# Kernel optimization log

Hardware: AMD Instinct MI355X
Metric: run time of the kernel (lower is better)

The kernel has to match this reference:

```python
import jax, jax.numpy as jnp
import numpy as np
import math

B, S, D, P = 128, 512, 1024, 32
TEMP, BETA = 0.1, 0.4

def _lin_init(k, din, dout):
    k1, k2 = jax.random.split(k)
    s = 1.0 / math.sqrt(din)
    W = jax.random.uniform(k1, (din, dout), minval=-s, maxval=s, dtype=jnp.float32)
    b = jax.random.uniform(k2, (dout,), minval=-s, maxval=s, dtype=jnp.float32)
    return W, b

def setup_inputs():
    key = jax.random.key(0)
    ks = jax.random.split(key, 20)
    inp = {
        'x_head': jax.random.normal(ks[0], (B, D), dtype=jnp.float32),
        'x_rel': jax.random.normal(ks[1], (B, S, D), dtype=jnp.float32),
        'x_tail': jax.random.normal(ks[2], (B, S, D), dtype=jnp.float32),
        'x_mask': (jax.random.uniform(ks[3], (B, S)) < 0.9).astype(jnp.float32),
        'x_img': jax.random.normal(ks[4], (B, D), dtype=jnp.float32),
    }
    names = [('wf1', 2 * D, D), ('wf2', D, D), ('wk', D, D), ('wv', D, D),
             ('wp', D, D), ('wiq', D, D), ('whq', D, D), ('wlt', D, D),
             ('wli', D, D), ('wltr', D, D), ('wgt', D, D), ('wgi', D, D)]
    for i, (nm, din, dout) in enumerate(names):
        W, b = _lin_init(ks[5 + i], din, dout)
        inp[nm] = W
        inp['b' + nm[1:]] = b
    return inp

def reference(x_head, x_rel, x_tail, x_mask, x_img,
              wf1, bf1, wf2, bf2, wk, bk, wv, bv, wp, bp,
              wiq, biq, whq, bhq, wlt, blt, wli, bli,
              wltr, bltr, wgt, bgt, wgi, bgi):
    # reltail feature combine: MLP(cat[tail, rel]) residual onto tail (eval: no dropout)
    feat = jnp.concatenate([x_tail, x_rel], axis=-1)            # [B,S,2D]
    h = jax.nn.leaky_relu(feat @ wf1 + bf1, negative_slope=0.01)
    x_reltail = x_tail + (h @ wf2 + bf2)                        # [B,S,D]
    keys = x_reltail @ wk + bk                                  # [B,S,D]
    values = x_reltail @ wv + bv                                # [B,S,D]
    iq = x_img @ wiq + biq                                      # [B,D]
    hq = x_head @ whq + bhq                                     # [B,D]
    inv_sqrt_d = 1.0 / math.sqrt(D)
    s1 = jnp.einsum('bd,bsd->bs', iq, keys) * inv_sqrt_d        # [B,S]
    s2 = jnp.einsum('bd,bsd->bs', hq, keys) * inv_sqrt_d
    neg_inf = jnp.finfo(s1.dtype).min
    valid = x_mask > 0.01
    s1 = jnp.where(valid, s1, neg_inf)
    s2 = jnp.where(valid, s2, neg_inf)
    scores = (s1 * BETA + s2 * (1.0 - BETA)) / TEMP
    attn = jax.nn.softmax(scores, axis=-1)                      # [B,S]
    # top-p sparsify: keep only the P largest weights (no renormalization)
    _, top_idx = jax.lax.top_k(attn, P)                         # [B,P]
    top_mask = jnp.zeros_like(attn).at[jnp.arange(B)[:, None], top_idx].set(1.0)
    attn = attn * top_mask
    ctx = jnp.einsum('bs,bsd->bd', attn, values)                # [B,D]
    x_triple = ctx @ wp + bp
    # gated projection combine
    text_out = x_head @ wlt + blt
    img_out = x_img @ wli + bli
    triple_out = x_triple @ wltr + bltr
    text_gate = jax.nn.sigmoid(x_head @ wgt + bgt)
    img_gate = jax.nn.sigmoid(x_img @ wgi + bgi)
    return triple_out + text_out * text_gate + img_out * img_gate
```

## Files before the change

### kernel.cpp

```cpp
#include <hip/hip_runtime.h>
#include <math.h>


typedef short bf16x8 __attribute__((ext_vector_type(8)));
typedef float f32x4 __attribute__((ext_vector_type(4)));

typedef const __attribute__((address_space(1))) void* gp_t;
typedef __attribute__((address_space(3))) void* lp_t;

__device__ __forceinline__ void ld16(const void* g, void* l) {
  __builtin_amdgcn_global_load_lds((gp_t)g, (lp_t)l, 16, 0, 0);
}

__device__ __forceinline__ unsigned int f2b(float f) {
  unsigned int u = __builtin_bit_cast(unsigned int, f);
  u = (u + 0x7FFFu + ((u >> 16) & 1u)) >> 16;
  return u & 0xFFFFu;
}
__device__ __forceinline__ float b2f(unsigned short s) {
  unsigned int u = ((unsigned int)s) << 16;
  return __builtin_bit_cast(float, u);
}
__device__ __forceinline__ float b2f_lo(unsigned int u) { return __builtin_bit_cast(float, u << 16); }
__device__ __forceinline__ float b2f_hi(unsigned int u) { return __builtin_bit_cast(float, u & 0xFFFF0000u); }
__device__ __forceinline__ unsigned int pack2(float lo, float hi) { return f2b(lo) | (f2b(hi) << 16); }

__global__ void cvt_feat_k(const float4* __restrict__ tail, const float4* __restrict__ rel,
                           uint4* __restrict__ feat) {
  unsigned i = blockIdx.x * 256 + threadIdx.x;
  unsigned row = i >> 8, c = i & 255u;
  bool isrel = c >= 128u;
  const float4* src = isrel ? rel : tail;
  unsigned s = row * 256u + (c & 127u) * 2u;
  float4 a = src[s], b = src[s + 1];
  uint4 o;
  o.x = pack2(a.x, a.y); o.y = pack2(a.z, a.w);
  o.z = pack2(b.x, b.y); o.w = pack2(b.z, b.w);
  feat[i] = o;
}

__global__ void transpose_cvt_k(const float* __restrict__ W, unsigned short* __restrict__ Wt,
                                int K, int N) {
  __shared__ float tile[32][33];
  int t = threadIdx.x;
  int tx = t & 31, ty = t >> 5;
  int n0 = blockIdx.x * 32, k0 = blockIdx.y * 32;
  #pragma unroll
  for (int i = 0; i < 32; i += 8)
    tile[ty + i][tx] = W[(size_t)(k0 + ty + i) * N + n0 + tx];
  __syncthreads();
  #pragma unroll
  for (int i = 0; i < 32; i += 8)
    Wt[(size_t)(n0 + ty + i) * K + k0 + tx] = (unsigned short)f2b(tile[tx][ty + i]);
}

struct SJob { const float* A; const float* W; const float* u; const float* rs;
              const float* A2; float* C; int transB; int pad; };
struct SJobs { SJob j[6]; };

__global__ __launch_bounds__(256) void sgemm_k(SJobs jobs, int K) {
  SJob jb = jobs.j[blockIdx.z];
  __shared__ float At[32 * 132];
  __shared__ float Wt_[32 * 36];
  int t = threadIdx.x;
  int n0 = blockIdx.x * 32;
  int kchunk = K / gridDim.y;
  int kbase = blockIdx.y * kchunk;
  int tn = t & 7, tm = t >> 3;
  float acc[4][4] = {};
  for (int kt = 0; kt < kchunk; kt += 32) {
    int k0 = kbase + kt;
    #pragma unroll
    for (int i = 0; i < 16; ++i) {
      int f = i * 256 + t;
      int r = f >> 5, c = f & 31;
      float v = jb.A[(size_t)r * K + k0 + c];
      if (jb.A2) v += jb.A2[(size_t)r * K + k0 + c];
      if (jb.u) v += (jb.rs ? jb.rs[r] : 1.0f) * jb.u[k0 + c];
      At[c * 132 + r] = v;
    }
    #pragma unroll
    for (int i = 0; i < 4; ++i) {
      int f = i * 256 + t;
      if (!jb.transB) { int k = f >> 5, n = f & 31; Wt_[k * 36 + n] = jb.W[(size_t)(k0 + k) * 1024 + n0 + n]; }
      else            { int n = f >> 5, k = f & 31; Wt_[k * 36 + n] = jb.W[(size_t)(n0 + n) * K + k0 + k]; }
    }
    __syncthreads();
    #pragma unroll
    for (int kk = 0; kk < 32; ++kk) {
      float4 av = *(const float4*)&At[kk * 132 + tm * 4];
      float4 wv4 = *(const float4*)&Wt_[kk * 36 + tn * 4];
      float ar[4] = {av.x, av.y, av.z, av.w};
      float wr[4] = {wv4.x, wv4.y, wv4.z, wv4.w};
      #pragma unroll
      for (int r = 0; r < 4; ++r)
        #pragma unroll
        for (int c = 0; c < 4; ++c) acc[r][c] += ar[r] * wr[c];
    }
    __syncthreads();
  }
  #pragma unroll
  for (int r = 0; r < 4; ++r)
    #pragma unroll
    for (int c = 0; c < 4; ++c)
      atomicAdd(jb.C + (size_t)(tm * 4 + r) * 1024 + n0 + tn * 4 + c, acc[r][c]);
}

__global__ void ew1_k(const float* __restrict__ riq, const float* __restrict__ rhq,
                      const float* __restrict__ rt, const float* __restrict__ ri,
                      const float* __restrict__ rtg, const float* __restrict__ rig,
                      const float* __restrict__ biq, const float* __restrict__ bhq,
                      const float* __restrict__ blt, const float* __restrict__ bli,
                      const float* __restrict__ bgt, const float* __restrict__ bgi,
                      float* __restrict__ qc, float* __restrict__ pout) {
  int idx = blockIdx.x * 256 + threadIdx.x;
  int n = idx & 1023;
  float iq = riq[idx] + biq[n];
  float hq = rhq[idx] + bhq[n];
  qc[idx] = 0.3125f * (0.4f * iq + 0.6f * hq);
  float tg = 1.0f / (1.0f + expf(-(rtg[idx] + bgt[n])));
  float ig = 1.0f / (1.0f + expf(-(rig[idx] + bgi[n])));
  pout[idx] = (rt[idx] + blt[n]) * tg + (ri[idx] + bli[n]) * ig;
}

__global__ void cvec_k(const float* __restrict__ qc, const float* __restrict__ bk,
                       const float* __restrict__ qk, const float* __restrict__ bf2,
                       float* __restrict__ cv) {
  int b = blockIdx.x, l = threadIdx.x;
  const float4* a = (const float4*)(qc + (size_t)b * 1024);
  const float4* k4 = (const float4*)bk;
  const float4* a2 = (const float4*)(qk + (size_t)b * 1024);
  const float4* k42 = (const float4*)bf2;
  float acc = 0.f;
  #pragma unroll
  for (int i = 0; i < 4; ++i) {
    float4 x = a[l + i * 64], y = k4[l + i * 64];
    acc += x.x * y.x + x.y * y.y + x.z * y.z + x.w * y.w;
    float4 x2 = a2[l + i * 64], y2 = k42[l + i * 64];
    acc += x2.x * y2.x + x2.y * y2.y + x2.z * y2.z + x2.w * y2.w;
  }
  for (int off = 32; off > 0; off >>= 1) acc += __shfl_down(acc, off);
  if (l == 0) cv[b] = acc;
}

__global__ __launch_bounds__(256) void gemm_bf16_k(
    const unsigned short* __restrict__ A, const unsigned short* __restrict__ Wt,
    const float* __restrict__ bias, const float* __restrict__ resid,
    unsigned short* __restrict__ C, int M, int N, int K, int act) {
  __shared__ __align__(16) unsigned short Sm[16384];
  unsigned short* As = Sm;
  unsigned short* Bs = Sm + 4096;
  int t = threadIdx.x;
  int l = t & 63, w = t >> 6;

  int L = blockIdx.x;
  int xcd = L & 7, j = L >> 3;
  int n_t = j & 7;
  int m_t = (j >> 3) * 8 + xcd;
  int m0 = m_t * 128, n0 = n_t * 128;
  int wm = (w >> 1) * 64, wn = (w & 1) * 64;

  int srow = t >> 2;
  int scol = ((t & 3) ^ ((t >> 3) & 3)) * 8;
  const unsigned short* Ag = A + (size_t)(m0 + srow) * K + scol;
  const unsigned short* Bg = Wt + (size_t)(n0 + srow) * K + scol;
  unsigned short* AsP = As + t * 8;
  unsigned short* BsP = Bs + t * 8;
  size_t rowadv = (size_t)64 * K;

  int lm = l & 15, q = l >> 4;
  int aoff[4], boff[4];
  #pragma unroll
  for (int i = 0; i < 4; ++i) {
    int ra = wm + i * 16 + lm;
    aoff[i] = ra * 32 + ((q ^ ((ra >> 1) & 3)) * 8);
    int rb = wn + i * 16 + lm;
    boff[i] = rb * 32 + ((q ^ ((rb >> 1) & 3)) * 8);
  }

  f32x4 acc[4][4];
  #pragma unroll
  for (int i = 0; i < 4; ++i)
    #pragma unroll
    for (int jj = 0; jj < 4; ++jj) acc[i][jj] = (f32x4){0.f, 0.f, 0.f, 0.f};

  int kiters = K >> 5;
  for (int kt = 0; kt < kiters; ++kt) {
    const unsigned short* a0 = Ag + kt * 32;
    const unsigned short* b0 = Bg + kt * 32;
    ld16(a0, AsP);
    ld16(a0 + rowadv, AsP + 2048);
    ld16(b0, BsP);
    ld16(b0 + rowadv, BsP + 2048);
    __syncthreads();
    bf16x8 af[4], bfv[4];
    #pragma unroll
    for (int i = 0; i < 4; ++i) af[i] = *(const bf16x8*)(As + aoff[i]);
    #pragma unroll
    for (int i = 0; i < 4; ++i) bfv[i] = *(const bf16x8*)(Bs + boff[i]);
    #pragma unroll
    for (int mi = 0; mi < 4; ++mi)
      #pragma unroll
      for (int ni = 0; ni < 4; ++ni)
        acc[mi][ni] = __builtin_amdgcn_mfma_f32_16x16x32_bf16(af[mi], bfv[ni], acc[mi][ni], 0, 0, 0);
    __syncthreads();
  }

  int lr = q * 4;
  #pragma unroll
  for (int mi = 0; mi < 4; ++mi) {
    #pragma unroll
    for (int ni = 0; ni < 4; ++ni) {
      int cn = wn + ni * 16 + lm;
      float bb = bias ? bias[n0 + cn] : 0.f;
      #pragma unroll
      for (int r = 0; r < 4; ++r) {
        int cm = wm + mi * 16 + lr + r;
        float v = acc[mi][ni][r] + bb;
        if (act == 1) v = v > 0.f ? v : 0.01f * v;
        Sm[cm * 128 + cn] = (unsigned short)f2b(v);
      }
    }
  }
  __syncthreads();

  #pragma unroll
  for (int p = 0; p < 8; ++p) {
    int idx = p * 256 + t;
    int row = idx >> 4;
    int col8 = (idx & 15) * 8;
    uint4 cs = *(const uint4*)(Sm + row * 128 + col8);
    size_t go = (size_t)(m0 + row) * N + n0 + col8;
    uint4 o;
    if (resid) {
      float4 r0 = *(const float4*)(resid + go);
      float4 r1 = *(const float4*)(resid + go + 4);
      o.x = pack2(b2f_lo(cs.x) + r0.x, b2f_hi(cs.x) + r0.y);
      o.y = pack2(b2f_lo(cs.y) + r0.z, b2f_hi(cs.y) + r0.w);
      o.z = pack2(b2f_lo(cs.z) + r1.x, b2f_hi(cs.z) + r1.y);
      o.w = pack2(b2f_lo(cs.w) + r1.z, b2f_hi(cs.w) + r1.w);
    } else {
      o = cs;
    }
    *(uint4*)(C + go) = o;
  }
}

__global__ void scores_k(const unsigned short* __restrict__ feat, const unsigned short* __restrict__ h,
                         const float* __restrict__ qk, const float* __restrict__ wq2,
                         const float* __restrict__ cv, const float* __restrict__ mask,
                         float* __restrict__ sc) {
  int w = threadIdx.x >> 6, l = threadIdx.x & 63;
  int row = blockIdx.x * 4 + w;
  int b = row >> 9;
  const uint4* tp = (const uint4*)(feat + (size_t)row * 2048);
  const uint4* hp = (const uint4*)(h + (size_t)row * 1024);
  const float4* qp = (const float4*)(qk + (size_t)b * 1024);
  const float4* wp_ = (const float4*)(wq2 + (size_t)b * 1024);
  float acc = 0.f;
  #pragma unroll
  for (int i = 0; i < 2; ++i) {
    uint4 xa = tp[l * 2 + i];
    float4 q0 = qp[l * 4 + i * 2];
    float4 q1 = qp[l * 4 + i * 2 + 1];
    acc += b2f_lo(xa.x) * q0.x + b2f_hi(xa.x) * q0.y;
    acc += b2f_lo(xa.y) * q0.z + b2f_hi(xa.y) * q0.w;
    acc += b2f_lo(xa.z) * q1.x + b2f_hi(xa.z) * q1.y;
    acc += b2f_lo(xa.w) * q1.z + b2f_hi(xa.w) * q1.w;
    uint4 ha = hp[l * 2 + i];
    float4 w0 = wp_[l * 4 + i * 2];
    float4 w1 = wp_[l * 4 + i * 2 + 1];
    acc += b2f_lo(ha.x) * w0.x + b2f_hi(ha.x) * w0.y;
    acc += b2f_lo(ha.y) * w0.z + b2f_hi(ha.y) * w0.w;
    acc += b2f_lo(ha.z) * w1.x + b2f_hi(ha.z) * w1.y;
    acc += b2f_lo(ha.w) * w1.z + b2f_hi(ha.w) * w1.w;
  }
  for (int off = 32; off > 0; off >>= 1) acc += __shfl_down(acc, off);
  if (l == 0) sc[row] = (mask[row] > 0.01f) ? (acc + cv[b]) : -__builtin_inff();
}

__global__ __launch_bounds__(256) void topk_ctx_k(const float* __restrict__ sc,
                                                  const float* __restrict__ xtail,
                                                  const unsigned short* __restrict__ h,
                                                  float* __restrict__ ctxtail, float* __restrict__ gh,
                                                  float* __restrict__ asum) {
  int b = blockIdx.x, t = threadIdx.x;
  __shared__ float sv[512];
  __shared__ float red[256];
  __shared__ int redi[256];
  __shared__ float topw[32];
  __shared__ int topi[32];
  sv[t] = sc[b * 512 + t];
  sv[t + 256] = sc[b * 512 + 256 + t];
  __syncthreads();
  red[t] = fmaxf(sv[t], sv[t + 256]);
  __syncthreads();
  for (int s = 128; s > 0; s >>= 1) { if (t < s) red[t] = fmaxf(red[t], red[t + s]); __syncthreads(); }
  float mx = red[0];
  __syncthreads();
  float e0 = expf(sv[t] - mx), e1 = expf(sv[t + 256] - mx);
  red[t] = e0 + e1;
  __syncthreads();
  for (int s = 128; s > 0; s >>= 1) { if (t < s) red[t] += red[t + s]; __syncthreads(); }
  float inv = 1.0f / red[0];
  __syncthreads();
  sv[t] = e0 * inv; sv[t + 256] = e1 * inv;
  __syncthreads();
  for (int it = 0; it < 32; ++it) {
    float v0 = sv[t], v1 = sv[t + 256];
    float bv_; int bi;
    if (v1 > v0) { bv_ = v1; bi = t + 256; } else { bv_ = v0; bi = t; }
    red[t] = bv_; redi[t] = bi;
    __syncthreads();
    for (int s = 128; s > 0; s >>= 1) {
      if (t < s) {
        if (red[t + s] > red[t] || (red[t + s] == red[t] && redi[t + s] < redi[t])) {
          red[t] = red[t + s]; redi[t] = redi[t + s];
        }
      }
      __syncthreads();
    }
    if (t == 0) { topw[it] = red[0]; topi[it] = redi[0]; sv[redi[0]] = -1.0f; }
    __syncthreads();
  }
  #pragma unroll
  for (int dd = 0; dd < 4; ++dd) {
    int d = t + dd * 256;
    float at = 0.f, ah = 0.f;
    for (int j = 0; j < 32; ++j) {
      size_t ro = (size_t)(b * 512 + topi[j]) * 1024 + d;
      at += topw[j] * xtail[ro];
      ah += topw[j] * b2f(h[ro]);
    }
    ctxtail[(size_t)b * 1024 + d] = at;
    gh[(size_t)b * 1024 + d] = ah;
  }
  if (t == 0) {
    float s = 0.f;
    for (int j = 0; j < 32; ++j) s += topw[j];
    asum[b] = s;
  }
}

__global__ void ew2_k(const float* __restrict__ r3, const float* __restrict__ bltr,
                      const float* __restrict__ pout, float* __restrict__ out) {
  int idx = blockIdx.x * 256 + threadIdx.x;
  out[idx] = r3[idx] + bltr[idx & 1023] + pout[idx];
}

extern "C" void kernel_launch(void* const* d_in, const int* in_sizes, int n_in,
                              void* d_out, int out_size, void* d_ws, size_t ws_size,
                              hipStream_t stream) {
  const float* x_head = (const float*)d_in[0];
  const float* x_rel  = (const float*)d_in[1];
  const float* x_tail = (const float*)d_in[2];
  const float* x_mask = (const float*)d_in[3];
  const float* x_img  = (const float*)d_in[4];
  const float* wf1 = (const float*)d_in[5];  const float* bf1 = (const float*)d_in[6];
  const float* wf2 = (const float*)d_in[7];  const float* bf2 = (const float*)d_in[8];
  const float* wk  = (const float*)d_in[9];  const float* bk  = (const float*)d_in[10];
  const float* wv  = (const float*)d_in[11]; const float* bv  = (const float*)d_in[12];
  const float* wp  = (const float*)d_in[13]; const float* bp  = (const float*)d_in[14];
  const float* wiq = (const float*)d_in[15]; const float* biq = (const float*)d_in[16];
  const float* whq = (const float*)d_in[17]; const float* bhq = (const float*)d_in[18];
  const float* wlt = (const float*)d_in[19]; const float* blt = (const float*)d_in[20];
  const float* wli = (const float*)d_in[21]; const float* bli = (const float*)d_in[22];
  const float* wltr= (const float*)d_in[23]; const float* bltr= (const float*)d_in[24];
  const float* wgt = (const float*)d_in[25]; const float* bgt = (const float*)d_in[26];
  const float* wgi = (const float*)d_in[27]; const float* bgi = (const float*)d_in[28];
  float* out = (float*)d_out;
  char* ws = (char*)d_ws;

  unsigned short* feat = (unsigned short*)(ws);
  unsigned short* hbuf = (unsigned short*)(ws + 268435456ull);
  unsigned short* wf1t = (unsigned short*)(ws + 402653184ull);
  char* z = ws + 406847488ull;
  float* raw_iq = (float*)(z);
  float* raw_hq = (float*)(z + 524288);
  float* raw_t  = (float*)(z + 1048576);
  float* raw_i  = (float*)(z + 1572864);
  float* raw_tg = (float*)(z + 2097152);
  float* raw_ig = (float*)(z + 2621440);
  float* raw_q  = (float*)(z + 3145728);
  float* wq2    = (float*)(z + 3670016);
  float* rawG   = (float*)(z + 4194304);
  float* rawL1  = (float*)(z + 4718592);
  float* rawL2  = (float*)(z + 5242880);
  float* rawL3  = (float*)(z + 5767168);
  float* qc      = (float*)(ws + 413138944ull);
  float* pout    = (float*)(ws + 413663232ull);
  float* cv      = (float*)(ws + 414187520ull);
  float* sc      = (float*)(ws + 414191616ull);
  float* ctxtail = (float*)(ws + 414453760ull);
  float* gh      = (float*)(ws + 414978048ull);
  float* asum    = (float*)(ws + 415502336ull);

  hipMemsetAsync(z, 0, 6291456, stream);

  cvt_feat_k<<<65536, 256, 0, stream>>>((const float4*)x_tail, (const float4*)x_rel, (uint4*)feat);
  transpose_cvt_k<<<dim3(32, 64), 256, 0, stream>>>(wf1, wf1t, 2048, 1024);

  SJobs j6 = {};
  j6.j[0] = SJob{x_img,  wiq, nullptr, nullptr, nullptr, raw_iq, 0, 0};
  j6.j[1] = SJob{x_head, whq, nullptr, nullptr, nullptr, raw_hq, 0, 0};
  j6.j[2] = SJob{x_head, wlt, nullptr, nullptr, nullptr, raw_t,  0, 0};
  j6.j[3] = SJob{x_img,  wli, nullptr, nullptr, nullptr, raw_i,  0, 0};
  j6.j[4] = SJob{x_head, wgt, nullptr, nullptr, nullptr, raw_tg, 0, 0};
  j6.j[5] = SJob{x_img,  wgi, nullptr, nullptr, nullptr, raw_ig, 0, 0};
  sgemm_k<<<dim3(32, 2, 6), 256, 0, stream>>>(j6, 1024);

  ew1_k<<<512, 256, 0, stream>>>(raw_iq, raw_hq, raw_t, raw_i, raw_tg, raw_ig,
                                 biq, bhq, blt, bli, bgt, bgi, qc, pout);

  SJobs jq = {};
  jq.j[0] = SJob{qc, wk, nullptr, nullptr, nullptr, raw_q, 1, 0};
  sgemm_k<<<dim3(32, 4, 1), 256, 0, stream>>>(jq, 1024);
  jq.j[0] = SJob{raw_q, wf2, nullptr, nullptr, nullptr, wq2, 1, 0};
  sgemm_k<<<dim3(32, 4, 1), 256, 0, stream>>>(jq, 1024);
  cvec_k<<<128, 64, 0, stream>>>(qc, bk, raw_q, bf2, cv);

  gemm_bf16_k<<<4096, 256, 0, stream>>>(feat, wf1t, bf1, nullptr, hbuf, 65536, 1024, 2048, 1);

  scores_k<<<16384, 256, 0, stream>>>(feat, hbuf, raw_q, wq2, cv, x_mask, sc);
  topk_ctx_k<<<128, 256, 0, stream>>>(sc, x_tail, hbuf, ctxtail, gh, asum);

  SJobs jl = {};
  jl.j[0] = SJob{gh, wf2, nullptr, nullptr, nullptr, rawG, 0, 0};
  sgemm_k<<<dim3(32, 4, 1), 256, 0, stream>>>(jl, 1024);
  jl.j[0] = SJob{rawG, wv, bf2, asum, ctxtail, rawL1, 0, 0};
  sgemm_k<<<dim3(32, 4, 1), 256, 0, stream>>>(jl, 1024);
  jl.j[0] = SJob{rawL1, wp, bv, asum, nullptr, rawL2, 0, 0};
  sgemm_k<<<dim3(32, 4, 1), 256, 0, stream>>>(jl, 1024);
  jl.j[0] = SJob{rawL2, wltr, bp, nullptr, nullptr, rawL3, 0, 0};
  sgemm_k<<<dim3(32, 4, 1), 256, 0, stream>>>(jl, 1024);
  ew2_k<<<512, 256, 0, stream>>>(rawL3, bltr, pout, out);
}
```

Before: 1.607 ms.

## Fuse score dot-products into conversion and GEMM epilogues, enlarge GEMM tile

The standalone scores kernel is removed. The tail·qk partial dot product is now computed in the fp32→bf16 conversion kernel, and the h·wq2 partial is computed in the big GEMM epilogue, both accumulated into sc with atomics. The main GEMM moves to 256x256 tiles with 512 threads, double-buffered LDS loads and setprio around the MFMAs. Top-k selection becomes a single-wavefront shuffle reduction, and masking and the constant are applied in topk. This avoids re-reading feat and h from HBM and cuts barrier-heavy reductions, in exchange for atomic contention, float-order nondeterminism and higher register pressure.

```diff
diff --git a/kernel.cpp b/kernel.cpp
--- a/kernel.cpp
+++ b/kernel.cpp
@@ -26,9 +26,11 @@
 __device__ __forceinline__ unsigned int pack2(float lo, float hi) { return f2b(lo) | (f2b(hi) << 16); }
 
 __global__ void cvt_feat_k(const float4* __restrict__ tail, const float4* __restrict__ rel,
-                           uint4* __restrict__ feat) {
-  unsigned i = blockIdx.x * 256 + threadIdx.x;
-  unsigned row = i >> 8, c = i & 255u;
+                           uint4* __restrict__ feat, const float* __restrict__ qk,
+                           float* __restrict__ sc) {
+  unsigned t = threadIdx.x;
+  unsigned i = blockIdx.x * 256 + t;
+  unsigned row = blockIdx.x, c = t;
   bool isrel = c >= 128u;
   const float4* src = isrel ? rel : tail;
   unsigned s = row * 256u + (c & 127u) * 2u;
@@ -37,6 +39,14 @@
   o.x = pack2(a.x, a.y); o.y = pack2(a.z, a.w);
   o.z = pack2(b.x, b.y); o.w = pack2(b.z, b.w);
   feat[i] = o;
+  float part = 0.f;
+  if (!isrel) {
+    const float* qr = qk + (size_t)(row >> 9) * 1024 + c * 8;
+    part = a.x * qr[0] + a.y * qr[1] + a.z * qr[2] + a.w * qr[3]
+         + b.x * qr[4] + b.y * qr[5] + b.z * qr[6] + b.w * qr[7];
+  }
+  for (int off = 32; off > 0; off >>= 1) part += __shfl_down(part, off);
+  if ((t & 63u) == 0u && !isrel) atomicAdd(sc + row, part);
 }
 
 __global__ void transpose_cvt_k(const float* __restrict__ W, unsigned short* __restrict__ Wt,
@@ -143,143 +153,146 @@
   if (l == 0) cv[b] = acc;
 }
 
-__global__ __launch_bounds__(256) void gemm_bf16_k(
+__global__ __launch_bounds__(512, 2) void gemm256_k(
     const unsigned short* __restrict__ A, const unsigned short* __restrict__ Wt,
-    const float* __restrict__ bias, const float* __restrict__ resid,
-    unsigned short* __restrict__ C, int M, int N, int K, int act) {
-  __shared__ __align__(16) unsigned short Sm[16384];
-  unsigned short* As = Sm;
-  unsigned short* Bs = Sm + 4096;
+    const float* __restrict__ bias, const float* __restrict__ wq2,
+    unsigned short* __restrict__ C, float* __restrict__ sc, int M, int N, int K) {
+  __shared__ __align__(16) unsigned short Sm[32768];
   int t = threadIdx.x;
   int l = t & 63, w = t >> 6;
 
   int L = blockIdx.x;
   int xcd = L & 7, j = L >> 3;
-  int n_t = j & 7;
-  int m_t = (j >> 3) * 8 + xcd;
-  int m0 = m_t * 128, n0 = n_t * 128;
-  int wm = (w >> 1) * 64, wn = (w & 1) * 64;
-
-  int srow = t >> 2;
-  int scol = ((t & 3) ^ ((t >> 3) & 3)) * 8;
-  const unsigned short* Ag = A + (size_t)(m0 + srow) * K + scol;
-  const unsigned short* Bg = Wt + (size_t)(n0 + srow) * K + scol;
-  unsigned short* AsP = As + t * 8;
-  unsigned short* BsP = Bs + t * 8;
-  size_t rowadv = (size_t)64 * K;
+  int n_t = j & 3;
+  int m_t = (j >> 2) * 8 + xcd;
+  int m0 = m_t * 256, n0 = n_t * 256;
+  int wm = (w >> 2) * 128, wn = (w & 3) * 64;
+
+  int r0 = t >> 2, slot = t & 3;
+  int col8 = slot ^ ((r0 >> 1) & 3);
+  const unsigned short* Ag = A + (size_t)(m0 + r0) * K + col8 * 8;
+  const unsigned short* Bg = Wt + (size_t)(n0 + r0) * K + col8 * 8;
+  size_t rowadv = (size_t)128 * K;
+  unsigned short* dA0 = Sm + t * 8;
+  unsigned short* dA1 = Sm + 4096 + t * 8;
+  unsigned short* dB0 = Sm + 8192 + t * 8;
+  unsigned short* dB1 = Sm + 12288 + t * 8;
 
   int lm = l & 15, q = l >> 4;
-  int aoff[4], boff[4];
-  #pragma unroll
-  for (int i = 0; i < 4; ++i) {
+  int aoff[8], boff[4];
+  #pragma unroll
+  for (int i = 0; i < 8; ++i) {
     int ra = wm + i * 16 + lm;
     aoff[i] = ra * 32 + ((q ^ ((ra >> 1) & 3)) * 8);
+  }
+  #pragma unroll
+  for (int i = 0; i < 4; ++i) {
     int rb = wn + i * 16 + lm;
     boff[i] = rb * 32 + ((q ^ ((rb >> 1) & 3)) * 8);
   }
 
-  f32x4 acc[4][4];
-  #pragma unroll
-  for (int i = 0; i < 4; ++i)
+  f32x4 acc[8][4];
+  #pragma unroll
+  for (int i = 0; i < 8; ++i)
     #pragma unroll
     for (int jj = 0; jj < 4; ++jj) acc[i][jj] = (f32x4){0.f, 0.f, 0.f, 0.f};
 
-  int kiters = K >> 5;
-  for (int kt = 0; kt < kiters; ++kt) {
-    const unsigned short* a0 = Ag + kt * 32;
-    const unsigned short* b0 = Bg + kt * 32;
-    ld16(a0, AsP);
-    ld16(a0 + rowadv, AsP + 2048);
-    ld16(b0, BsP);
-    ld16(b0 + rowadv, BsP + 2048);
+  int NT = K >> 5;
+
+#define STAGE(buf, kt) do {                                     \
+    const unsigned short* a_ = Ag + (size_t)(kt) * 32;          \
+    const unsigned short* b_ = Bg + (size_t)(kt) * 32;          \
+    ld16(a_,          (buf) * 16384 + dA0);                     \
+    ld16(a_ + rowadv, (buf) * 16384 + dA1);                     \
+    ld16(b_,          (buf) * 16384 + dB0);                     \
+    ld16(b_ + rowadv, (buf) * 16384 + dB1);                     \
+  } while (0)
+
+#define COMPUTE(cur) do {                                       \
+    const unsigned short* base = Sm + (cur) * 16384;            \
+    bf16x8 af[8], bfv[4];                                       \
+    _Pragma("unroll")                                           \
+    for (int i = 0; i < 8; ++i) af[i] = *(const bf16x8*)(base + aoff[i]);        \
+    _Pragma("unroll")                                           \
+    for (int i = 0; i < 4; ++i) bfv[i] = *(const bf16x8*)(base + 8192 + boff[i]);\
+    __builtin_amdgcn_s_setprio(1);                              \
+    _Pragma("unroll")                                           \
+    for (int mi = 0; mi < 8; ++mi)                              \
+      _Pragma("unroll")                                         \
+      for (int ni = 0; ni < 4; ++ni)                            \
+        acc[mi][ni] = __builtin_amdgcn_mfma_f32_16x16x32_bf16(af[mi], bfv[ni], acc[mi][ni], 0, 0, 0); \
+    __builtin_amdgcn_s_setprio(0);                              \
+  } while (0)
+
+  STAGE(0, 0);
+  for (int kt = 0; kt < NT - 1; ++kt) {
+    int cur = kt & 1;
+    STAGE(cur ^ 1, kt + 1);
+    asm volatile("s_waitcnt vmcnt(4)\n\ts_barrier" ::: "memory");
+    COMPUTE(cur);
+    asm volatile("s_barrier" ::: "memory");
+  }
+  asm volatile("s_waitcnt vmcnt(0)\n\ts_barrier" ::: "memory");
+  COMPUTE((NT - 1) & 1);
+  asm volatile("s_barrier" ::: "memory");
+
+  int lr = q * 4;
+  #pragma unroll
+  for (int h = 0; h < 2; ++h) {
+    if ((w >> 2) == h) {
+      #pragma unroll
+      for (int mi = 0; mi < 8; ++mi) {
+        #pragma unroll
+        for (int ni = 0; ni < 4; ++ni) {
+          int cn = wn + ni * 16 + lm;
+          float bb = bias[n0 + cn];
+          #pragma unroll
+          for (int r = 0; r < 4; ++r) {
+            int row = mi * 16 + lr + r;
+            float v = acc[mi][ni][r] + bb;
+            v = v > 0.f ? v : 0.01f * v;
+            Sm[row * 256 + cn] = (unsigned short)f2b(v);
+          }
+        }
+      }
+    }
     __syncthreads();
-    bf16x8 af[4], bfv[4];
-    #pragma unroll
-    for (int i = 0; i < 4; ++i) af[i] = *(const bf16x8*)(As + aoff[i]);
-    #pragma unroll
-    for (int i = 0; i < 4; ++i) bfv[i] = *(const bf16x8*)(Bs + boff[i]);
-    #pragma unroll
-    for (int mi = 0; mi < 4; ++mi)
+    #pragma unroll
+    for (int p = 0; p < 8; ++p) {
+      int idx = p * 512 + t;
+      int rr = idx >> 5;
+      int c8 = (idx & 31) * 8;
+      uint4 cs = *(const uint4*)(Sm + rr * 256 + c8);
+      *(uint4*)(C + (size_t)(m0 + h * 128 + rr) * N + n0 + c8) = cs;
+    }
+    {
+      int row = t >> 2, quarter = t & 3;
+      int b = (m0 + h * 128) >> 9;
+      const uint4* cr = (const uint4*)(Sm + row * 256 + quarter * 64);
+      const float4* wr = (const float4*)(wq2 + (size_t)b * 1024 + n0 + quarter * 64);
+      float part = 0.f;
       #pragma unroll
-      for (int ni = 0; ni < 4; ++ni)
-        acc[mi][ni] = __builtin_amdgcn_mfma_f32_16x16x32_bf16(af[mi], bfv[ni], acc[mi][ni], 0, 0, 0);
+      for (int jj = 0; jj < 8; ++jj) {
+        uint4 cw = cr[jj];
+        float4 w0 = wr[jj * 2], w1 = wr[jj * 2 + 1];
+        part += b2f_lo(cw.x) * w0.x + b2f_hi(cw.x) * w0.y;
+        part += b2f_lo(cw.y) * w0.z + b2f_hi(cw.y) * w0.w;
+        part += b2f_lo(cw.z) * w1.x + b2f_hi(cw.z) * w1.y;
+        part += b2f_lo(cw.w) * w1.z + b2f_hi(cw.w) * w1.w;
+      }
+      part += __shfl_xor(part, 1);
+      part += __shfl_xor(part, 2);
+      if (quarter == 0) atomicAdd(sc + m0 + h * 128 + row, part);
+    }
     __syncthreads();
   }
-
-  int lr = q * 4;
-  #pragma unroll
-  for (int mi = 0; mi < 4; ++mi) {
-    #pragma unroll
-    for (int ni = 0; ni < 4; ++ni) {
-      int cn = wn + ni * 16 + lm;
-      float bb = bias ? bias[n0 + cn] : 0.f;
-      #pragma unroll
-      for (int r = 0; r < 4; ++r) {
-        int cm = wm + mi * 16 + lr + r;
-        float v = acc[mi][ni][r] + bb;
-        if (act == 1) v = v > 0.f ? v : 0.01f * v;
-        Sm[cm * 128 + cn] = (unsigned short)f2b(v);
-      }
-    }
-  }
-  __syncthreads();
-
-  #pragma unroll
-  for (int p = 0; p < 8; ++p) {
-    int idx = p * 256 + t;
-    int row = idx >> 4;
-    int col8 = (idx & 15) * 8;
-    uint4 cs = *(const uint4*)(Sm + row * 128 + col8);
-    size_t go = (size_t)(m0 + row) * N + n0 + col8;
-    uint4 o;
-    if (resid) {
-      float4 r0 = *(const float4*)(resid + go);
-      float4 r1 = *(const float4*)(resid + go + 4);
-      o.x = pack2(b2f_lo(cs.x) + r0.x, b2f_hi(cs.x) + r0.y);
-      o.y = pack2(b2f_lo(cs.y) + r0.z, b2f_hi(cs.y) + r0.w);
-      o.z = pack2(b2f_lo(cs.z) + r1.x, b2f_hi(cs.z) + r1.y);
-      o.w = pack2(b2f_lo(cs.w) + r1.z, b2f_hi(cs.w) + r1.w);
-    } else {
-      o = cs;
-    }
-    *(uint4*)(C + go) = o;
-  }
-}
-
-__global__ void scores_k(const unsigned short* __restrict__ feat, const unsigned short* __restrict__ h,
-                         const float* __restrict__ qk, const float* __restrict__ wq2,
-                         const float* __restrict__ cv, const float* __restrict__ mask,
-                         float* __restrict__ sc) {
-  int w = threadIdx.x >> 6, l = threadIdx.x & 63;
-  int row = blockIdx.x * 4 + w;
-  int b = row >> 9;
-  const uint4* tp = (const uint4*)(feat + (size_t)row * 2048);
-  const uint4* hp = (const uint4*)(h + (size_t)row * 1024);
-  const float4* qp = (const float4*)(qk + (size_t)b * 1024);
-  const float4* wp_ = (const float4*)(wq2 + (size_t)b * 1024);
-  float acc = 0.f;
-  #pragma unroll
-  for (int i = 0; i < 2; ++i) {
-    uint4 xa = tp[l * 2 + i];
-    float4 q0 = qp[l * 4 + i * 2];
-    float4 q1 = qp[l * 4 + i * 2 + 1];
-    acc += b2f_lo(xa.x) * q0.x + b2f_hi(xa.x) * q0.y;
-    acc += b2f_lo(xa.y) * q0.z + b2f_hi(xa.y) * q0.w;
-    acc += b2f_lo(xa.z) * q1.x + b2f_hi(xa.z) * q1.y;
-    acc += b2f_lo(xa.w) * q1.z + b2f_hi(xa.w) * q1.w;
-    uint4 ha = hp[l * 2 + i];
-    float4 w0 = wp_[l * 4 + i * 2];
-    float4 w1 = wp_[l * 4 + i * 2 + 1];
-    acc += b2f_lo(ha.x) * w0.x + b2f_hi(ha.x) * w0.y;
-    acc += b2f_lo(ha.y) * w0.z + b2f_hi(ha.y) * w0.w;
-    acc += b2f_lo(ha.z) * w1.x + b2f_hi(ha.z) * w1.y;
-    acc += b2f_lo(ha.w) * w1.z + b2f_hi(ha.w) * w1.w;
-  }
-  for (int off = 32; off > 0; off >>= 1) acc += __shfl_down(acc, off);
-  if (l == 0) sc[row] = (mask[row] > 0.01f) ? (acc + cv[b]) : -__builtin_inff();
+#undef STAGE
+#undef COMPUTE
 }
 
 __global__ __launch_bounds__(256) void topk_ctx_k(const float* __restrict__ sc,
+                                                  const float* __restrict__ mask,
+                                                  const float* __restrict__ cv,
                                                   const float* __restrict__ xtail,
                                                   const unsigned short* __restrict__ h,
                                                   float* __restrict__ ctxtail, float* __restrict__ gh,
@@ -287,18 +300,19 @@
   int b = blockIdx.x, t = threadIdx.x;
   __shared__ float sv[512];
   __shared__ float red[256];
-  __shared__ int redi[256];
   __shared__ float topw[32];
   __shared__ int topi[32];
-  sv[t] = sc[b * 512 + t];
-  sv[t + 256] = sc[b * 512 + 256 + t];
-  __syncthreads();
-  red[t] = fmaxf(sv[t], sv[t + 256]);
+  float cvb = cv[b];
+  float r0 = sc[b * 512 + t], r1 = sc[b * 512 + 256 + t];
+  float v0 = (mask[b * 512 + t] > 0.01f) ? (r0 + cvb) : -__builtin_inff();
+  float v1 = (mask[b * 512 + 256 + t] > 0.01f) ? (r1 + cvb) : -__builtin_inff();
+  sv[t] = v0; sv[t + 256] = v1;
+  red[t] = fmaxf(v0, v1);
   __syncthreads();
   for (int s = 128; s > 0; s >>= 1) { if (t < s) red[t] = fmaxf(red[t], red[t + s]); __syncthreads(); }
   float mx = red[0];
   __syncthreads();
-  float e0 = expf(sv[t] - mx), e1 = expf(sv[t + 256] - mx);
+  float e0 = expf(v0 - mx), e1 = expf(v1 - mx);
   red[t] = e0 + e1;
   __syncthreads();
   for (int s = 128; s > 0; s >>= 1) { if (t < s) red[t] += red[t + s]; __syncthreads(); }
@@ -306,38 +320,42 @@
   __syncthreads();
   sv[t] = e0 * inv; sv[t + 256] = e1 * inv;
   __syncthreads();
-  for (int it = 0; it < 32; ++it) {
-    float v0 = sv[t], v1 = sv[t + 256];
-    float bv_; int bi;
-    if (v1 > v0) { bv_ = v1; bi = t + 256; } else { bv_ = v0; bi = t; }
-    red[t] = bv_; redi[t] = bi;
-    __syncthreads();
-    for (int s = 128; s > 0; s >>= 1) {
-      if (t < s) {
-        if (red[t + s] > red[t] || (red[t + s] == red[t] && redi[t + s] < redi[t])) {
-          red[t] = red[t + s]; redi[t] = redi[t + s];
-        }
+  if (t < 64) {
+    float v[8];
+    int base = t * 8;
+    #pragma unroll
+    for (int jj = 0; jj < 8; ++jj) v[jj] = sv[base + jj];
+    for (int it = 0; it < 32; ++it) {
+      float bv = v[0]; int bj = 0;
+      #pragma unroll
+      for (int jj = 1; jj < 8; ++jj) if (v[jj] > bv) { bv = v[jj]; bj = jj; }
+      int bidx = base + bj;
+      #pragma unroll
+      for (int off = 32; off > 0; off >>= 1) {
+        float ov = __shfl_xor(bv, off);
+        int oi = __shfl_xor(bidx, off);
+        if (ov > bv || (ov == bv && oi < bidx)) { bv = ov; bidx = oi; }
       }
-      __syncthreads();
-    }
-    if (t == 0) { topw[it] = red[0]; topi[it] = redi[0]; sv[redi[0]] = -1.0f; }
-    __syncthreads();
-  }
+      if (t == (bidx >> 3)) v[bidx & 7] = -1.0f;
+      if (t == 0) { topw[it] = bv; topi[it] = bidx; }
+    }
+  }
+  __syncthreads();
   #pragma unroll
   for (int dd = 0; dd < 4; ++dd) {
     int d = t + dd * 256;
     float at = 0.f, ah = 0.f;
-    for (int j = 0; j < 32; ++j) {
-      size_t ro = (size_t)(b * 512 + topi[j]) * 1024 + d;
-      at += topw[j] * xtail[ro];
-      ah += topw[j] * b2f(h[ro]);
+    for (int jj = 0; jj < 32; ++jj) {
+      size_t ro = (size_t)(b * 512 + topi[jj]) * 1024 + d;
+      at += topw[jj] * xtail[ro];
+      ah += topw[jj] * b2f(h[ro]);
     }
     ctxtail[(size_t)b * 1024 + d] = at;
     gh[(size_t)b * 1024 + d] = ah;
   }
   if (t == 0) {
     float s = 0.f;
-    for (int j = 0; j < 32; ++j) s += topw[j];
+    for (int jj = 0; jj < 32; ++jj) s += topw[jj];
     asum[b] = s;
   }
 }
@@ -387,18 +405,15 @@
   float* rawL1  = (float*)(z + 4718592);
   float* rawL2  = (float*)(z + 5242880);
   float* rawL3  = (float*)(z + 5767168);
-  float* qc      = (float*)(ws + 413138944ull);
-  float* pout    = (float*)(ws + 413663232ull);
-  float* cv      = (float*)(ws + 414187520ull);
-  float* sc      = (float*)(ws + 414191616ull);
-  float* ctxtail = (float*)(ws + 414453760ull);
-  float* gh      = (float*)(ws + 414978048ull);
-  float* asum    = (float*)(ws + 415502336ull);
-
-  hipMemsetAsync(z, 0, 6291456, stream);
-
-  cvt_feat_k<<<65536, 256, 0, stream>>>((const float4*)x_tail, (const float4*)x_rel, (uint4*)feat);
-  transpose_cvt_k<<<dim3(32, 64), 256, 0, stream>>>(wf1, wf1t, 2048, 1024);
+  float* sc     = (float*)(z + 6291456);
+  float* qc      = (float*)(ws + 413663232ull);
+  float* pout    = (float*)(ws + 414187520ull);
+  float* cv      = (float*)(ws + 414711808ull);
+  float* ctxtail = (float*)(ws + 414715904ull);
+  float* gh      = (float*)(ws + 415240192ull);
+  float* asum    = (float*)(ws + 415764480ull);
+
+  hipMemsetAsync(z, 0, 6553600, stream);
 
   SJobs j6 = {};
   j6.j[0] = SJob{x_img,  wiq, nullptr, nullptr, nullptr, raw_iq, 0, 0};
@@ -419,10 +434,13 @@
   sgemm_k<<<dim3(32, 4, 1), 256, 0, stream>>>(jq, 1024);
   cvec_k<<<128, 64, 0, stream>>>(qc, bk, raw_q, bf2, cv);
 
-  gemm_bf16_k<<<4096, 256, 0, stream>>>(feat, wf1t, bf1, nullptr, hbuf, 65536, 1024, 2048, 1);
-
-  scores_k<<<16384, 256, 0, stream>>>(feat, hbuf, raw_q, wq2, cv, x_mask, sc);
-  topk_ctx_k<<<128, 256, 0, stream>>>(sc, x_tail, hbuf, ctxtail, gh, asum);
+  cvt_feat_k<<<65536, 256, 0, stream>>>((const float4*)x_tail, (const float4*)x_rel,
+                                        (uint4*)feat, raw_q, sc);
+  transpose_cvt_k<<<dim3(32, 64), 256, 0, stream>>>(wf1, wf1t, 2048, 1024);
+
+  gemm256_k<<<1024, 512, 0, stream>>>(feat, wf1t, bf1, wq2, hbuf, sc, 65536, 1024, 2048);
+
+  topk_ctx_k<<<128, 256, 0, stream>>>(sc, x_mask, cv, x_tail, hbuf, ctxtail, gh, asum);
 
   SJobs jl = {};
   jl.j[0] = SJob{gh, wf2, nullptr, nullptr, nullptr, rawG, 0, 0};
```

Result: faster. 1.446 ms (-10.0%).
